# Kernel optimization log

Measured on AMD Instinct MI355X. Metric: run time of the kernel, lower is better.

Reference implementation:

```python
import jax, jax.numpy as jnp
import numpy as np

N = 100000
E = 1600000
IN_C = 128
HID = 128


def setup_inputs() -> dict:
    key = jax.random.key(0)
    ks = jax.random.split(key, 16)
    x = jax.random.normal(ks[0], (N, IN_C), dtype=jnp.float32)
    edge_index = jax.random.randint(ks[1], (2, E), 0, N, dtype=jnp.int64)

    def lin(k, fan_in, fan_out):
        kw, kb = jax.random.split(k)
        bound = 1.0 / np.sqrt(fan_in)
        w = jax.random.uniform(kw, (fan_in, fan_out), minval=-bound, maxval=bound, dtype=jnp.float32)
        b = jax.random.uniform(kb, (fan_out,), minval=-bound, maxval=bound, dtype=jnp.float32)
        return w, b

    w0a, b0a = lin(ks[2], IN_C, HID)
    w0b, b0b = lin(ks[3], HID, HID)
    w1a, b1a = lin(ks[4], HID, HID)
    w1b, b1b = lin(ks[5], HID, HID)
    w2a, b2a = lin(ks[6], HID, HID)
    w2b, b2b = lin(ks[7], HID, HID)
    lin_w, lin_b = lin(ks[8], HID, 1)
    return {
        "x": x, "edge_index": edge_index,
        "w0a": w0a, "b0a": b0a, "w0b": w0b, "b0b": b0b,
        "w1a": w1a, "b1a": b1a, "w1b": w1b, "b1b": b1b,
        "w2a": w2a, "b2a": b2a, "w2b": w2b, "b2b": b2b,
        "lin_w": lin_w, "lin_b": lin_b,
    }


def _gin_conv(x, src, dst, wa, ba, wb, bb):
    # scatter-add neighbor sum: agg[i] = sum_{(j,i) in edges} x[j]  (eps = 0)
    agg = jax.ops.segment_sum(x[src], dst, num_segments=N)
    h = x + agg
    h = jax.nn.relu(h @ wa + ba)
    return h @ wb + bb


def reference(x, edge_index, w0a, b0a, w0b, b0b, w1a, b1a, w1b, b1b,
              w2a, b2a, w2b, b2b, lin_w, lin_b):
    src, dst = edge_index[0], edge_index[1]
    # dropout is identity in eval mode
    h = jax.nn.elu(_gin_conv(x, src, dst, w0a, b0a, w0b, b0b))
    h = jax.nn.elu(_gin_conv(h, src, dst, w1a, b1a, w1b, b1b))
    h = jax.nn.elu(_gin_conv(h, src, dst, w2a, b2a, w2b, b2b))
    out = jax.nn.sigmoid(h @ lin_w + lin_b)
    return out.squeeze(-1)  # [N]
```

## Files before the change

### kernel.cpp

```cpp
#include <hip/hip_runtime.h>
#include <hip/hip_bf16.h>
#include <math.h>

#define NN 100000
#define CC 128
#define EE 1600000
#define EPT 8
#define FCHUNK (256 * EPT)
#define NCHUNKS ((EE + FCHUNK - 1) / FCHUNK)
#define NB_E NCHUNKS
#define WB 512
#define WSHIFT 9
#define NBUCK ((NN + WB - 1) / WB)

typedef short  bf16x8 __attribute__((ext_vector_type(8)));
typedef float  f32x4  __attribute__((ext_vector_type(4)));
typedef float  f32x4v __attribute__((ext_vector_type(4)));
typedef unsigned short u16x8 __attribute__((ext_vector_type(8)));

#define WPAD 136
#define TP   136
#define MLPB 256
#define MLPW 8

__device__ __forceinline__ ushort f2bf(float f) {
    __hip_bfloat16 h = __float2bfloat16(f);
    return __builtin_bit_cast(ushort, h);
}
__device__ __forceinline__ float bf2f(ushort u) {
    return __builtin_bit_cast(float, ((unsigned int)u) << 16);
}


__global__ void __launch_bounds__(256) bucket_hist(
    const int* __restrict__ dst, int* __restrict__ cnt)
{
    __shared__ int h[NBUCK];
    for (int i = threadIdx.x; i < NBUCK; i += 256) h[i] = 0;
    __syncthreads();
    int base = blockIdx.x * FCHUNK + threadIdx.x * EPT;
    if (base + EPT <= EE) {
        int4 d0 = *(const int4*)&dst[base];
        int4 d1 = *(const int4*)&dst[base + 4];
        int dd[8] = {d0.x, d0.y, d0.z, d0.w, d1.x, d1.y, d1.z, d1.w};
#pragma unroll
        for (int i = 0; i < 8; ++i) atomicAdd(&h[dd[i] >> WSHIFT], 1);
    } else {
        for (int i = 0; i < EPT; ++i) {
            int e = base + i;
            if (e < EE) atomicAdd(&h[dst[e] >> WSHIFT], 1);
        }
    }
    __syncthreads();
    for (int i = threadIdx.x; i < NBUCK; i += 256)
        cnt[i * NB_E + blockIdx.x] = h[i];
}

__global__ void __launch_bounds__(256) scan_cnt(
    int* __restrict__ cnt, int* __restrict__ total)
{
    __shared__ int wsum[4];
    int row = blockIdx.x;
    int* p = cnt + row * NB_E;
    int tid = threadIdx.x, lane = tid & 63, wid = tid >> 6;
    int v[4], s = 0;
#pragma unroll
    for (int j = 0; j < 4; ++j) {
        int idx = tid * 4 + j;
        v[j] = (idx < NB_E) ? p[idx] : 0;
        s += v[j];
    }
    int inc = s;
#pragma unroll
    for (int off = 1; off < 64; off <<= 1) {
        int n = __shfl_up(inc, off);
        if (lane >= off) inc += n;
    }
    if (lane == 63) wsum[wid] = inc;
    __syncthreads();
    int wofs = 0;
#pragma unroll
    for (int w = 0; w < 4; ++w)
        if (w < wid) wofs += wsum[w];
    int run = wofs + inc - s;
#pragma unroll
    for (int j = 0; j < 4; ++j) {
        int idx = tid * 4 + j;
        if (idx < NB_E) p[idx] = run;
        run += v[j];
    }
    if (tid == 255) total[row] = run;
}

__global__ void scan_base(const int* __restrict__ total,
                          int* __restrict__ bucketBase, int* __restrict__ rowptr)
{
    int lane = threadIdx.x;
    int v[4], s = 0;
#pragma unroll
    for (int j = 0; j < 4; ++j) {
        int idx = lane * 4 + j;
        v[j] = (idx < NBUCK) ? total[idx] : 0;
        s += v[j];
    }
    int inc = s;
#pragma unroll
    for (int off = 1; off < 64; off <<= 1) {
        int n = __shfl_up(inc, off);
        if (lane >= off) inc += n;
    }
    int run = inc - s;
#pragma unroll
    for (int j = 0; j < 4; ++j) {
        int idx = lane * 4 + j;
        if (idx < NBUCK) bucketBase[idx] = run;
        run += v[j];
    }
    if (lane == 63) { bucketBase[NBUCK] = EE; rowptr[NN] = EE; }
}

__global__ void __launch_bounds__(256) bucket_scatter(
    const int* __restrict__ src, const int* __restrict__ dst,
    const int* __restrict__ cntEx, const int* __restrict__ bucketBase,
    unsigned int* __restrict__ pairs)
{
    __shared__ int h[NBUCK];
    __shared__ int bOfs[NBUCK];
    for (int i = threadIdx.x; i < NBUCK; i += 256) {
        h[i] = 0;
        bOfs[i] = bucketBase[i] + cntEx[i * NB_E + blockIdx.x];
    }
    __syncthreads();
    int base = blockIdx.x * FCHUNK + threadIdx.x * EPT;
    if (base + EPT <= EE) {
        int4 d0 = *(const int4*)&dst[base];
        int4 d1 = *(const int4*)&dst[base + 4];
        int4 s0 = *(const int4*)&src[base];
        int4 s1 = *(const int4*)&src[base + 4];
        int dd[8] = {d0.x, d0.y, d0.z, d0.w, d1.x, d1.y, d1.z, d1.w};
        int ss[8] = {s0.x, s0.y, s0.z, s0.w, s1.x, s1.y, s1.z, s1.w};
#pragma unroll
        for (int i = 0; i < 8; ++i) {
            int d = dd[i];
            int k = d >> WSHIFT;
            int r = atomicAdd(&h[k], 1);
            pairs[bOfs[k] + r] = ((unsigned)ss[i] << WSHIFT) | (unsigned)(d & (WB - 1));
        }
    } else {
        for (int i = 0; i < EPT; ++i) {
            int e = base + i;
            if (e < EE) {
                int d = dst[e];
                int k = d >> WSHIFT;
                int r = atomicAdd(&h[k], 1);
                pairs[bOfs[k] + r] = ((unsigned)src[e] << WSHIFT) | (unsigned)(d & (WB - 1));
            }
        }
    }
}

__global__ void __launch_bounds__(256) csr_build(
    const unsigned int* __restrict__ pairs, const int* __restrict__ bucketBase,
    int* __restrict__ rowptr, int* __restrict__ col)
{
    __shared__ int cnt[WB];
    __shared__ int ofs[WB];
    __shared__ int wsum[4];
    int k = blockIdx.x;
    int tid = threadIdx.x, lane = tid & 63, wid = tid >> 6;
    int nodeBase = k * WB;
    int nNodes = NN - nodeBase; if (nNodes > WB) nNodes = WB;
    for (int i = tid; i < WB; i += 256) cnt[i] = 0;
    __syncthreads();
    int beg = bucketBase[k], end = bucketBase[k + 1];
    for (int e = beg + tid; e < end; e += 256)
        atomicAdd(&cnt[pairs[e] & (WB - 1)], 1);
    __syncthreads();
    int a = cnt[2 * tid], b = cnt[2 * tid + 1];
    int s = a + b;
    int inc = s;
#pragma unroll
    for (int off = 1; off < 64; off <<= 1) {
        int n = __shfl_up(inc, off);
        if (lane >= off) inc += n;
    }
    if (lane == 63) wsum[wid] = inc;
    __syncthreads();
    int wofs = 0;
#pragma unroll
    for (int w = 0; w < 4; ++w)
        if (w < wid) wofs += wsum[w];
    int excl = wofs + inc - s;
    ofs[2 * tid] = excl;
    ofs[2 * tid + 1] = excl + a;
    __syncthreads();
    for (int i = tid; i < nNodes; i += 256)
        rowptr[nodeBase + i] = beg + ofs[i];
    __syncthreads();
    for (int e = beg + tid; e < end; e += 256) {
        unsigned p = pairs[e];
        int dl = p & (WB - 1);
        int r = atomicAdd(&ofs[dl], 1);
        col[beg + r] = (int)(p >> WSHIFT);
    }
}

__global__ void __launch_bounds__(256) convert_x_kernel(
    const float* __restrict__ x, ushort* __restrict__ xb)
{
    int i = blockIdx.x * 256 + threadIdx.x;
    f32x4v v = __builtin_nontemporal_load((const f32x4v*)x + i);
    ushort4 o;
    o.x = f2bf(v[0]); o.y = f2bf(v[1]); o.z = f2bf(v[2]); o.w = f2bf(v[3]);
    ((ushort4*)xb)[i] = o;
}

__global__ void __launch_bounds__(256) convert_w6_kernel(
    const float* __restrict__ w0, const float* __restrict__ w1,
    const float* __restrict__ w2, const float* __restrict__ w3,
    const float* __restrict__ w4, const float* __restrict__ w5,
    ushort* __restrict__ wt)
{
    int i = blockIdx.x * 256 + threadIdx.x;
    int mat = i >> 14;
    int rem = i & 16383;
    int k = rem >> 7, n = rem & 127;
    const float* w = (mat == 0) ? w0 : (mat == 1) ? w1 : (mat == 2) ? w2
                   : (mat == 3) ? w3 : (mat == 4) ? w4 : w5;
    wt[mat * 16384 + n * 128 + k] = f2bf(w[k * 128 + n]);
}

__global__ void __launch_bounds__(256) gather_agg(
    const ushort* __restrict__ hin, const int* __restrict__ rowptr,
    const int* __restrict__ col, ushort* __restrict__ agg)
{
    const int grp    = threadIdx.x >> 4;
    const int lane16 = threadIdx.x & 15;
    const int gbase  = (threadIdx.x & 63) & 48;
    const int n = blockIdx.x * 16 + grp;
    const u16x8* hp = (const u16x8*)hin;

    u16x8 self = hp[n * 16 + lane16];
    float s0[8], s1[8], s2[8], s3[8];
#pragma unroll
    for (int k = 0; k < 8; ++k) {
        s0[k] = bf2f(self[k]); s1[k] = 0.f; s2[k] = 0.f; s3[k] = 0.f;
    }

    int beg = rowptr[n], end = rowptr[n + 1];
    while (beg < end) {
        int take = end - beg;
        if (take > 16) take = 16;
        int ci = (lane16 < take) ? col[beg + lane16] : 0;
        int j = 0;
        for (; j + 4 <= take; j += 4) {
            int n0 = __shfl(ci, gbase + j + 0);
            int n1 = __shfl(ci, gbase + j + 1);
            int n2 = __shfl(ci, gbase + j + 2);
            int n3 = __shfl(ci, gbase + j + 3);
            u16x8 a0 = hp[n0 * 16 + lane16];
            u16x8 a1 = hp[n1 * 16 + lane16];
            u16x8 a2 = hp[n2 * 16 + lane16];
            u16x8 a3 = hp[n3 * 16 + lane16];
#pragma unroll
            for (int k = 0; k < 8; ++k) {
                s0[k] += bf2f(a0[k]); s1[k] += bf2f(a1[k]);
                s2[k] += bf2f(a2[k]); s3[k] += bf2f(a3[k]);
            }
        }
        for (; j < take; ++j) {
            int n0 = __shfl(ci, gbase + j);
            u16x8 a0 = hp[n0 * 16 + lane16];
#pragma unroll
            for (int k = 0; k < 8; ++k) s0[k] += bf2f(a0[k]);
        }
        beg += take;
    }

    bf16x8 o;
#pragma unroll
    for (int k = 0; k < 8; ++k) o[k] = (short)f2bf(s0[k] + s1[k] + s2[k] + s3[k]);
    *(bf16x8*)&((ushort*)agg)[n * CC + lane16 * 8] = o;
}

template <bool FUSE_HEAD>
__global__ void __launch_bounds__(512, 2) mlp_persist(
    const ushort* __restrict__ hin,
    const ushort* __restrict__ waT, const float* __restrict__ ba,
    const ushort* __restrict__ wbT, const float* __restrict__ bb,
    ushort* __restrict__ hout,
    const float* __restrict__ lw, const float* __restrict__ lb,
    float* __restrict__ out)
{
    __shared__ ushort WaS[CC * WPAD];
    __shared__ ushort WbS[CC * WPAD];
    __shared__ ushort Tt[MLPW][16 * TP];
    __shared__ float  baS[CC], bbS[CC], lwS[CC];

    const int tid = threadIdx.x;

    for (int i = tid; i < CC * 16; i += 512) {
        int row = i >> 4, ch = i & 15;
        *(bf16x8*)&WaS[row * WPAD + ch * 8] = *(const bf16x8*)&waT[row * CC + ch * 8];
        *(bf16x8*)&WbS[row * WPAD + ch * 8] = *(const bf16x8*)&wbT[row * CC + ch * 8];
    }
    if (tid < CC)                    baS[tid]          = ba[tid];
    else if (tid < 2 * CC)           bbS[tid - CC]     = bb[tid - CC];
    else if (FUSE_HEAD && tid < 3 * CC) lwS[tid - 2 * CC] = lw[tid - 2 * CC];
    __syncthreads();

    const int wave = tid >> 6;
    const int lane = tid & 63;
    const int quad = lane >> 4;
    const int l16  = lane & 15;
    ushort* T = Tt[wave];
    const int nTiles = NN / 16;
    const int stride = MLPB * MLPW;

    int wv = blockIdx.x * MLPW + wave;
    if (wv >= nTiles) return;

    const int fq4 = quad * 4;
    float lbv = FUSE_HEAD ? lb[0] : 0.f;

    bf16x8 af[4];
#pragma unroll
    for (int kk = 0; kk < 4; ++kk)
        af[kk] = *(const bf16x8*)&hin[(wv * 16 + l16) * CC + kk * 32 + quad * 8];

    while (true) {
        const int wrow0 = wv * 16;
        const int wnext = wv + stride;

        bf16x8 afn[4];
        if (wnext < nTiles) {
#pragma unroll
            for (int kk = 0; kk < 4; ++kk)
                afn[kk] = *(const bf16x8*)&hin[(wnext * 16 + l16) * CC + kk * 32 + quad * 8];
        }

        ushort* Trow = &T[l16 * TP];

#pragma unroll
        for (int nt = 0; nt < 8; ++nt) {
            f32x4 a = *(const f32x4*)&baS[nt * 16 + fq4];
#pragma unroll
            for (int kk = 0; kk < 4; ++kk) {
                bf16x8 wfrag = *(const bf16x8*)&WaS[(nt * 16 + l16) * WPAD + kk * 32 + quad * 8];
                a = __builtin_amdgcn_mfma_f32_16x16x32_bf16(wfrag, af[kk], a, 0, 0, 0);
            }
            ushort4 pk;
            pk.x = f2bf(fmaxf(a[0], 0.f));
            pk.y = f2bf(fmaxf(a[1], 0.f));
            pk.z = f2bf(fmaxf(a[2], 0.f));
            pk.w = f2bf(fmaxf(a[3], 0.f));
            *(ushort4*)&Trow[nt * 16 + fq4] = pk;
        }
        __builtin_amdgcn_sched_barrier(0);

        bf16x8 tf[4];
#pragma unroll
        for (int kk = 0; kk < 4; ++kk)
            tf[kk] = *(const bf16x8*)&Trow[kk * 32 + quad * 8];
        __builtin_amdgcn_sched_barrier(0);

        if (FUSE_HEAD) {
            float part = 0.f;
#pragma unroll
            for (int nt = 0; nt < 8; ++nt) {
                f32x4 a2 = *(const f32x4*)&bbS[nt * 16 + fq4];
#pragma unroll
                for (int kk = 0; kk < 4; ++kk) {
                    bf16x8 wfrag = *(const bf16x8*)&WbS[(nt * 16 + l16) * WPAD + kk * 32 + quad * 8];
                    a2 = __builtin_amdgcn_mfma_f32_16x16x32_bf16(wfrag, tf[kk], a2, 0, 0, 0);
                }
                f32x4 lw4 = *(const f32x4*)&lwS[nt * 16 + fq4];
#pragma unroll
                for (int r = 0; r < 4; ++r) {
                    float v = a2[r];
                    v = v > 0.f ? v : expm1f(v);
                    part += v * lw4[r];
                }
            }
            part += __shfl_xor(part, 16);
            part += __shfl_xor(part, 32);
            if (lane < 16) {
                float z = part + lbv;
                out[wrow0 + l16] = 1.f / (1.f + expf(-z));
            }
        } else {
#pragma unroll
            for (int nt = 0; nt < 8; ++nt) {
                f32x4 a2 = *(const f32x4*)&bbS[nt * 16 + fq4];
#pragma unroll
                for (int kk = 0; kk < 4; ++kk) {
                    bf16x8 wfrag = *(const bf16x8*)&WbS[(nt * 16 + l16) * WPAD + kk * 32 + quad * 8];
                    a2 = __builtin_amdgcn_mfma_f32_16x16x32_bf16(wfrag, tf[kk], a2, 0, 0, 0);
                }
                ushort4 pk;
#pragma unroll
                for (int r = 0; r < 4; ++r) {
                    float v = a2[r];
                    v = v > 0.f ? v : expm1f(v);
                    ((ushort*)&pk)[r] = f2bf(v);
                }
                *(ushort4*)&Trow[nt * 16 + fq4] = pk;
            }
#pragma unroll
            for (int i = 0; i < 4; ++i) {
                int r = i * 4 + quad;
                bf16x8 o = *(const bf16x8*)&T[r * TP + l16 * 8];
                *(bf16x8*)&hout[(wrow0 + r) * CC + l16 * 8] = o;
            }
        }

        if (wnext >= nTiles) break;
        wv = wnext;
#pragma unroll
        for (int kk = 0; kk < 4; ++kk) af[kk] = afn[kk];
    }
}

extern "C" void kernel_launch(void* const* d_in, const int* in_sizes, int n_in,
                              void* d_out, int out_size, void* d_ws, size_t ws_size,
                              hipStream_t stream) {
    const float* x   = (const float*)d_in[0];
    const int*   ei  = (const int*)d_in[1];
    const int*   src = ei;
    const int*   dst = ei + EE;
    const float* w0a = (const float*)d_in[2];
    const float* b0a = (const float*)d_in[3];
    const float* w0b = (const float*)d_in[4];
    const float* b0b = (const float*)d_in[5];
    const float* w1a = (const float*)d_in[6];
    const float* b1a = (const float*)d_in[7];
    const float* w1b = (const float*)d_in[8];
    const float* b1b = (const float*)d_in[9];
    const float* w2a = (const float*)d_in[10];
    const float* b2a = (const float*)d_in[11];
    const float* w2b = (const float*)d_in[12];
    const float* b2b = (const float*)d_in[13];
    const float* lw  = (const float*)d_in[14];
    const float* lb  = (const float*)d_in[15];
    float* outp = (float*)d_out;

    ushort* xb  = (ushort*)d_ws;
    ushort* hbA = xb + (size_t)NN * CC;
    ushort* agg = hbA + (size_t)NN * CC;
    ushort* wT  = agg + (size_t)NN * CC;
    int* col    = (int*)(wT + 6 * CC * CC);
    int* rowptr = col + EE;

    unsigned int* pairs = (unsigned int*)agg;
    int* cnt        = (int*)(pairs + EE);
    int* total      = cnt + NBUCK * NB_E;
    int* bucketBase = total + NBUCK;

    ushort* w0aT = wT;
    ushort* w0bT = wT + 1 * CC * CC;
    ushort* w1aT = wT + 2 * CC * CC;
    ushort* w1bT = wT + 3 * CC * CC;
    ushort* w2aT = wT + 4 * CC * CC;
    ushort* w2bT = wT + 5 * CC * CC;

    const int gatherBlocks = NN / 16;
    const int cvtXBlocks   = (NN * CC / 4) / 256;

    convert_x_kernel<<<cvtXBlocks, 256, 0, stream>>>(x, xb);
    convert_w6_kernel<<<6 * 64, 256, 0, stream>>>(w0a, w0b, w1a, w1b, w2a, w2b, wT);

    bucket_hist<<<NB_E, 256, 0, stream>>>(dst, cnt);
    scan_cnt<<<NBUCK, 256, 0, stream>>>(cnt, total);
    scan_base<<<1, 64, 0, stream>>>(total, bucketBase, rowptr);
    bucket_scatter<<<NB_E, 256, 0, stream>>>(src, dst, cnt, bucketBase, pairs);
    csr_build<<<NBUCK, 256, 0, stream>>>(pairs, bucketBase, rowptr, col);

    gather_agg<<<gatherBlocks, 256, 0, stream>>>(xb, rowptr, col, agg);
    mlp_persist<false><<<MLPB, 512, 0, stream>>>(agg, w0aT, b0a, w0bT, b0b, hbA,
                                                 nullptr, nullptr, nullptr);
    gather_agg<<<gatherBlocks, 256, 0, stream>>>(hbA, rowptr, col, agg);
    mlp_persist<false><<<MLPB, 512, 0, stream>>>(agg, w1aT, b1a, w1bT, b1b, xb,
                                                 nullptr, nullptr, nullptr);
    gather_agg<<<gatherBlocks, 256, 0, stream>>>(xb, rowptr, col, agg);
    mlp_persist<true><<<MLPB, 512, 0, stream>>>(agg, w2aT, b2a, w2bT, b2b, nullptr,
                                                lw, lb, outp);
}
```

Measured before the change: 418.7 us.

## Fuse neighbor gather-aggregation with per-layer MLP into one kernel

Merges the gather_agg kernel and the persistent MLP kernel into a single gin_layer kernel. Each 256-thread block aggregates 16 nodes into LDS, then its four waves each compute two output column tiles of both MFMA matmuls, reading weights straight from global memory (L2-cached) instead of staging them in LDS. This removes the bf16 agg write and re-read to global memory and three kernel launches. In exchange, every block re-fetches the full weight matrices from cache, and there are more block-level barriers per tile.

```diff
diff --git a/kernel.cpp b/kernel.cpp
--- a/kernel.cpp
+++ b/kernel.cpp
@@ -18,10 +18,7 @@
 typedef float  f32x4v __attribute__((ext_vector_type(4)));
 typedef unsigned short u16x8 __attribute__((ext_vector_type(8)));
 
-#define WPAD 136
 #define TP   136
-#define MLPB 256
-#define MLPW 8
 
 __device__ __forceinline__ ushort f2bf(float f) {
     __hip_bfloat16 h = __float2bfloat16(f);
@@ -230,194 +227,156 @@
     wt[mat * 16384 + n * 128 + k] = f2bf(w[k * 128 + n]);
 }
 
-__global__ void __launch_bounds__(256) gather_agg(
+template <bool FUSE_HEAD>
+__global__ void __launch_bounds__(256, 4) gin_layer(
     const ushort* __restrict__ hin, const int* __restrict__ rowptr,
-    const int* __restrict__ col, ushort* __restrict__ agg)
-{
-    const int grp    = threadIdx.x >> 4;
-    const int lane16 = threadIdx.x & 15;
-    const int gbase  = (threadIdx.x & 63) & 48;
-    const int n = blockIdx.x * 16 + grp;
-    const u16x8* hp = (const u16x8*)hin;
-
-    u16x8 self = hp[n * 16 + lane16];
-    float s0[8], s1[8], s2[8], s3[8];
-#pragma unroll
-    for (int k = 0; k < 8; ++k) {
-        s0[k] = bf2f(self[k]); s1[k] = 0.f; s2[k] = 0.f; s3[k] = 0.f;
-    }
-
-    int beg = rowptr[n], end = rowptr[n + 1];
-    while (beg < end) {
-        int take = end - beg;
-        if (take > 16) take = 16;
-        int ci = (lane16 < take) ? col[beg + lane16] : 0;
-        int j = 0;
-        for (; j + 4 <= take; j += 4) {
-            int n0 = __shfl(ci, gbase + j + 0);
-            int n1 = __shfl(ci, gbase + j + 1);
-            int n2 = __shfl(ci, gbase + j + 2);
-            int n3 = __shfl(ci, gbase + j + 3);
-            u16x8 a0 = hp[n0 * 16 + lane16];
-            u16x8 a1 = hp[n1 * 16 + lane16];
-            u16x8 a2 = hp[n2 * 16 + lane16];
-            u16x8 a3 = hp[n3 * 16 + lane16];
-#pragma unroll
-            for (int k = 0; k < 8; ++k) {
-                s0[k] += bf2f(a0[k]); s1[k] += bf2f(a1[k]);
-                s2[k] += bf2f(a2[k]); s3[k] += bf2f(a3[k]);
-            }
-        }
-        for (; j < take; ++j) {
-            int n0 = __shfl(ci, gbase + j);
-            u16x8 a0 = hp[n0 * 16 + lane16];
-#pragma unroll
-            for (int k = 0; k < 8; ++k) s0[k] += bf2f(a0[k]);
-        }
-        beg += take;
-    }
-
-    bf16x8 o;
-#pragma unroll
-    for (int k = 0; k < 8; ++k) o[k] = (short)f2bf(s0[k] + s1[k] + s2[k] + s3[k]);
-    *(bf16x8*)&((ushort*)agg)[n * CC + lane16 * 8] = o;
-}
-
-template <bool FUSE_HEAD>
-__global__ void __launch_bounds__(512, 2) mlp_persist(
-    const ushort* __restrict__ hin,
+    const int* __restrict__ col,
     const ushort* __restrict__ waT, const float* __restrict__ ba,
     const ushort* __restrict__ wbT, const float* __restrict__ bb,
     ushort* __restrict__ hout,
     const float* __restrict__ lw, const float* __restrict__ lb,
     float* __restrict__ out)
 {
-    __shared__ ushort WaS[CC * WPAD];
-    __shared__ ushort WbS[CC * WPAD];
-    __shared__ ushort Tt[MLPW][16 * TP];
-    __shared__ float  baS[CC], bbS[CC], lwS[CC];
+    __shared__ ushort T0[16][TP];
+    __shared__ ushort T1[16][TP];
+    __shared__ float  headP[4][16];
 
     const int tid = threadIdx.x;
 
-    for (int i = tid; i < CC * 16; i += 512) {
-        int row = i >> 4, ch = i & 15;
-        *(bf16x8*)&WaS[row * WPAD + ch * 8] = *(const bf16x8*)&waT[row * CC + ch * 8];
-        *(bf16x8*)&WbS[row * WPAD + ch * 8] = *(const bf16x8*)&wbT[row * CC + ch * 8];
-    }
-    if (tid < CC)                    baS[tid]          = ba[tid];
-    else if (tid < 2 * CC)           bbS[tid - CC]     = bb[tid - CC];
-    else if (FUSE_HEAD && tid < 3 * CC) lwS[tid - 2 * CC] = lw[tid - 2 * CC];
+    {
+        const int grp  = tid >> 4;
+        const int g16  = tid & 15;
+        const int gbase = (tid & 63) & 48;
+        const int n = blockIdx.x * 16 + grp;
+        const u16x8* hp = (const u16x8*)hin;
+
+        u16x8 self = hp[n * 16 + g16];
+        float s0[8], s1[8], s2[8], s3[8];
+#pragma unroll
+        for (int k = 0; k < 8; ++k) {
+            s0[k] = bf2f(self[k]); s1[k] = 0.f; s2[k] = 0.f; s3[k] = 0.f;
+        }
+
+        int beg = rowptr[n], end = rowptr[n + 1];
+        while (beg < end) {
+            int take = end - beg;
+            if (take > 16) take = 16;
+            int ci = (g16 < take) ? col[beg + g16] : 0;
+            int j = 0;
+            for (; j + 4 <= take; j += 4) {
+                int n0 = __shfl(ci, gbase + j + 0);
+                int n1 = __shfl(ci, gbase + j + 1);
+                int n2 = __shfl(ci, gbase + j + 2);
+                int n3 = __shfl(ci, gbase + j + 3);
+                u16x8 a0 = hp[n0 * 16 + g16];
+                u16x8 a1 = hp[n1 * 16 + g16];
+                u16x8 a2 = hp[n2 * 16 + g16];
+                u16x8 a3 = hp[n3 * 16 + g16];
+#pragma unroll
+                for (int k = 0; k < 8; ++k) {
+                    s0[k] += bf2f(a0[k]); s1[k] += bf2f(a1[k]);
+                    s2[k] += bf2f(a2[k]); s3[k] += bf2f(a3[k]);
+                }
+            }
+            for (; j < take; ++j) {
+                int n0 = __shfl(ci, gbase + j);
+                u16x8 a0 = hp[n0 * 16 + g16];
+#pragma unroll
+                for (int k = 0; k < 8; ++k) s0[k] += bf2f(a0[k]);
+            }
+            beg += take;
+        }
+
+        bf16x8 o;
+#pragma unroll
+        for (int k = 0; k < 8; ++k) o[k] = (short)f2bf(s0[k] + s1[k] + s2[k] + s3[k]);
+        *(bf16x8*)&T0[grp][g16 * 8] = o;
+    }
     __syncthreads();
 
     const int wave = tid >> 6;
     const int lane = tid & 63;
     const int quad = lane >> 4;
     const int l16  = lane & 15;
-    ushort* T = Tt[wave];
-    const int nTiles = NN / 16;
-    const int stride = MLPB * MLPW;
-
-    int wv = blockIdx.x * MLPW + wave;
-    if (wv >= nTiles) return;
-
-    const int fq4 = quad * 4;
-    float lbv = FUSE_HEAD ? lb[0] : 0.f;
+    const int fq4  = quad * 4;
 
     bf16x8 af[4];
 #pragma unroll
     for (int kk = 0; kk < 4; ++kk)
-        af[kk] = *(const bf16x8*)&hin[(wv * 16 + l16) * CC + kk * 32 + quad * 8];
-
-    while (true) {
-        const int wrow0 = wv * 16;
-        const int wnext = wv + stride;
-
-        bf16x8 afn[4];
-        if (wnext < nTiles) {
-#pragma unroll
-            for (int kk = 0; kk < 4; ++kk)
-                afn[kk] = *(const bf16x8*)&hin[(wnext * 16 + l16) * CC + kk * 32 + quad * 8];
-        }
-
-        ushort* Trow = &T[l16 * TP];
-
-#pragma unroll
-        for (int nt = 0; nt < 8; ++nt) {
-            f32x4 a = *(const f32x4*)&baS[nt * 16 + fq4];
+        af[kk] = *(const bf16x8*)&T0[l16][kk * 32 + quad * 8];
+
+#pragma unroll
+    for (int t = 0; t < 2; ++t) {
+        const int nt = wave * 2 + t;
+        f32x4 a = *(const f32x4*)&ba[nt * 16 + fq4];
+#pragma unroll
+        for (int kk = 0; kk < 4; ++kk) {
+            bf16x8 wfrag = *(const bf16x8*)&waT[(nt * 16 + l16) * CC + kk * 32 + quad * 8];
+            a = __builtin_amdgcn_mfma_f32_16x16x32_bf16(wfrag, af[kk], a, 0, 0, 0);
+        }
+        ushort4 pk;
+        pk.x = f2bf(fmaxf(a[0], 0.f));
+        pk.y = f2bf(fmaxf(a[1], 0.f));
+        pk.z = f2bf(fmaxf(a[2], 0.f));
+        pk.w = f2bf(fmaxf(a[3], 0.f));
+        *(ushort4*)&T1[l16][nt * 16 + fq4] = pk;
+    }
+    __syncthreads();
+
+    bf16x8 tf[4];
+#pragma unroll
+    for (int kk = 0; kk < 4; ++kk)
+        tf[kk] = *(const bf16x8*)&T1[l16][kk * 32 + quad * 8];
+
+    if (FUSE_HEAD) {
+        float part = 0.f;
+#pragma unroll
+        for (int t = 0; t < 2; ++t) {
+            const int nt = wave * 2 + t;
+            f32x4 a2 = *(const f32x4*)&bb[nt * 16 + fq4];
 #pragma unroll
             for (int kk = 0; kk < 4; ++kk) {
-                bf16x8 wfrag = *(const bf16x8*)&WaS[(nt * 16 + l16) * WPAD + kk * 32 + quad * 8];
-                a = __builtin_amdgcn_mfma_f32_16x16x32_bf16(wfrag, af[kk], a, 0, 0, 0);
+                bf16x8 wfrag = *(const bf16x8*)&wbT[(nt * 16 + l16) * CC + kk * 32 + quad * 8];
+                a2 = __builtin_amdgcn_mfma_f32_16x16x32_bf16(wfrag, tf[kk], a2, 0, 0, 0);
+            }
+            f32x4 lw4 = *(const f32x4*)&lw[nt * 16 + fq4];
+#pragma unroll
+            for (int r = 0; r < 4; ++r) {
+                float v = a2[r];
+                v = v > 0.f ? v : expm1f(v);
+                part += v * lw4[r];
+            }
+        }
+        part += __shfl_xor(part, 16);
+        part += __shfl_xor(part, 32);
+        if (lane < 16) headP[wave][l16] = part;
+        __syncthreads();
+        if (tid < 16) {
+            float z = headP[0][tid] + headP[1][tid] + headP[2][tid] + headP[3][tid] + lb[0];
+            out[blockIdx.x * 16 + tid] = 1.f / (1.f + expf(-z));
+        }
+    } else {
+#pragma unroll
+        for (int t = 0; t < 2; ++t) {
+            const int nt = wave * 2 + t;
+            f32x4 a2 = *(const f32x4*)&bb[nt * 16 + fq4];
+#pragma unroll
+            for (int kk = 0; kk < 4; ++kk) {
+                bf16x8 wfrag = *(const bf16x8*)&wbT[(nt * 16 + l16) * CC + kk * 32 + quad * 8];
+                a2 = __builtin_amdgcn_mfma_f32_16x16x32_bf16(wfrag, tf[kk], a2, 0, 0, 0);
             }
             ushort4 pk;
-            pk.x = f2bf(fmaxf(a[0], 0.f));
-            pk.y = f2bf(fmaxf(a[1], 0.f));
-            pk.z = f2bf(fmaxf(a[2], 0.f));
-            pk.w = f2bf(fmaxf(a[3], 0.f));
-            *(ushort4*)&Trow[nt * 16 + fq4] = pk;
-        }
-        __builtin_amdgcn_sched_barrier(0);
-
-        bf16x8 tf[4];
-#pragma unroll
-        for (int kk = 0; kk < 4; ++kk)
-            tf[kk] = *(const bf16x8*)&Trow[kk * 32 + quad * 8];
-        __builtin_amdgcn_sched_barrier(0);
-
-        if (FUSE_HEAD) {
-            float part = 0.f;
-#pragma unroll
-            for (int nt = 0; nt < 8; ++nt) {
-                f32x4 a2 = *(const f32x4*)&bbS[nt * 16 + fq4];
-#pragma unroll
-                for (int kk = 0; kk < 4; ++kk) {
-                    bf16x8 wfrag = *(const bf16x8*)&WbS[(nt * 16 + l16) * WPAD + kk * 32 + quad * 8];
-                    a2 = __builtin_amdgcn_mfma_f32_16x16x32_bf16(wfrag, tf[kk], a2, 0, 0, 0);
-                }
-                f32x4 lw4 = *(const f32x4*)&lwS[nt * 16 + fq4];
-#pragma unroll
-                for (int r = 0; r < 4; ++r) {
-                    float v = a2[r];
-                    v = v > 0.f ? v : expm1f(v);
-                    part += v * lw4[r];
-                }
-            }
-            part += __shfl_xor(part, 16);
-            part += __shfl_xor(part, 32);
-            if (lane < 16) {
-                float z = part + lbv;
-                out[wrow0 + l16] = 1.f / (1.f + expf(-z));
-            }
-        } else {
-#pragma unroll
-            for (int nt = 0; nt < 8; ++nt) {
-                f32x4 a2 = *(const f32x4*)&bbS[nt * 16 + fq4];
-#pragma unroll
-                for (int kk = 0; kk < 4; ++kk) {
-                    bf16x8 wfrag = *(const bf16x8*)&WbS[(nt * 16 + l16) * WPAD + kk * 32 + quad * 8];
-                    a2 = __builtin_amdgcn_mfma_f32_16x16x32_bf16(wfrag, tf[kk], a2, 0, 0, 0);
-                }
-                ushort4 pk;
-#pragma unroll
-                for (int r = 0; r < 4; ++r) {
-                    float v = a2[r];
-                    v = v > 0.f ? v : expm1f(v);
-                    ((ushort*)&pk)[r] = f2bf(v);
-                }
-                *(ushort4*)&Trow[nt * 16 + fq4] = pk;
-            }
-#pragma unroll
-            for (int i = 0; i < 4; ++i) {
-                int r = i * 4 + quad;
-                bf16x8 o = *(const bf16x8*)&T[r * TP + l16 * 8];
-                *(bf16x8*)&hout[(wrow0 + r) * CC + l16 * 8] = o;
-            }
-        }
-
-        if (wnext >= nTiles) break;
-        wv = wnext;
-#pragma unroll
-        for (int kk = 0; kk < 4; ++kk) af[kk] = afn[kk];
+#pragma unroll
+            for (int r = 0; r < 4; ++r) {
+                float v = a2[r];
+                v = v > 0.f ? v : expm1f(v);
+                ((ushort*)&pk)[r] = f2bf(v);
+            }
+            *(ushort4*)&T0[l16][nt * 16 + fq4] = pk;
+        }
+        __syncthreads();
+        *(bf16x8*)&hout[(blockIdx.x * 16 + (tid >> 4)) * CC + (tid & 15) * 8] =
+            *(const bf16x8*)&T0[tid >> 4][(tid & 15) * 8];
     }
 }
 
@@ -446,12 +405,12 @@
 
     ushort* xb  = (ushort*)d_ws;
     ushort* hbA = xb + (size_t)NN * CC;
-    ushort* agg = hbA + (size_t)NN * CC;
-    ushort* wT  = agg + (size_t)NN * CC;
+    ushort* scr = hbA + (size_t)NN * CC;
+    ushort* wT  = scr + (size_t)NN * CC;
     int* col    = (int*)(wT + 6 * CC * CC);
     int* rowptr = col + EE;
 
-    unsigned int* pairs = (unsigned int*)agg;
+    unsigned int* pairs = (unsigned int*)scr;
     int* cnt        = (int*)(pairs + EE);
     int* total      = cnt + NBUCK * NB_E;
     int* bucketBase = total + NBUCK;
@@ -463,8 +422,8 @@
     ushort* w2aT = wT + 4 * CC * CC;
     ushort* w2bT = wT + 5 * CC * CC;
 
-    const int gatherBlocks = NN / 16;
-    const int cvtXBlocks   = (NN * CC / 4) / 256;
+    const int layerBlocks = NN / 16;
+    const int cvtXBlocks  = (NN * CC / 4) / 256;
 
     convert_x_kernel<<<cvtXBlocks, 256, 0, stream>>>(x, xb);
     convert_w6_kernel<<<6 * 64, 256, 0, stream>>>(w0a, w0b, w1a, w1b, w2a, w2b, wT);
@@ -475,13 +434,10 @@
     bucket_scatter<<<NB_E, 256, 0, stream>>>(src, dst, cnt, bucketBase, pairs);
     csr_build<<<NBUCK, 256, 0, stream>>>(pairs, bucketBase, rowptr, col);
 
-    gather_agg<<<gatherBlocks, 256, 0, stream>>>(xb, rowptr, col, agg);
-    mlp_persist<false><<<MLPB, 512, 0, stream>>>(agg, w0aT, b0a, w0bT, b0b, hbA,
-                                                 nullptr, nullptr, nullptr);
-    gather_agg<<<gatherBlocks, 256, 0, stream>>>(hbA, rowptr, col, agg);
-    mlp_persist<false><<<MLPB, 512, 0, stream>>>(agg, w1aT, b1a, w1bT, b1b, xb,
-                                                 nullptr, nullptr, nullptr);
-    gather_agg<<<gatherBlocks, 256, 0, stream>>>(xb, rowptr, col, agg);
-    mlp_persist<true><<<MLPB, 512, 0, stream>>>(agg, w2aT, b2a, w2bT, b2b, nullptr,
-                                                lw, lb, outp);
-}
+    gin_layer<false><<<layerBlocks, 256, 0, stream>>>(
+        xb, rowptr, col, w0aT, b0a, w0bT, b0b, hbA, nullptr, nullptr, nullptr);
+    gin_layer<false><<<layerBlocks, 256, 0, stream>>>(
+        hbA, rowptr, col, w1aT, b1a, w1bT, b1b, xb, nullptr, nullptr, nullptr);
+    gin_layer<true><<<layerBlocks, 256, 0, stream>>>(
+        xb, rowptr, col, w2aT, b2a, w2bT, b2b, nullptr, lw, lb, outp);
+}
```

Result: slower. 441.9 us (+5.5%).

## Fuse bucket histogram and scatter using fixed-capacity buckets with global atomics

Applied to the files above, without the earlier changes.

Replaces the histogram, per-block count scan and scatter passes with one kernel. It reserves per-bucket space through global atomics into fixed-capacity (PCAP) bucket slots, then scans the bucket totals for the CSR row offsets. This removes two kernel launches and one pass over dst. It relies on no bucket exceeding PCAP edges, which holds for uniform random inputs but could overflow on skewed graphs. The gather loop also gets an 8-wide unroll and a launch_bounds occupancy hint.

```diff
diff --git a/kernel.cpp b/kernel.cpp
--- a/kernel.cpp
+++ b/kernel.cpp
@@ -12,6 +12,7 @@
 #define WB 512
 #define WSHIFT 9
 #define NBUCK ((NN + WB - 1) / WB)
+#define PCAP 9216
 
 typedef short  bf16x8 __attribute__((ext_vector_type(8)));
 typedef float  f32x4  __attribute__((ext_vector_type(4)));
@@ -32,135 +33,94 @@
 }
 
 
-__global__ void __launch_bounds__(256) bucket_hist(
-    const int* __restrict__ dst, int* __restrict__ cnt)
-{
-    __shared__ int h[NBUCK];
-    for (int i = threadIdx.x; i < NBUCK; i += 256) h[i] = 0;
-    __syncthreads();
-    int base = blockIdx.x * FCHUNK + threadIdx.x * EPT;
-    if (base + EPT <= EE) {
-        int4 d0 = *(const int4*)&dst[base];
-        int4 d1 = *(const int4*)&dst[base + 4];
-        int dd[8] = {d0.x, d0.y, d0.z, d0.w, d1.x, d1.y, d1.z, d1.w};
-#pragma unroll
-        for (int i = 0; i < 8; ++i) atomicAdd(&h[dd[i] >> WSHIFT], 1);
-    } else {
-        for (int i = 0; i < EPT; ++i) {
-            int e = base + i;
-            if (e < EE) atomicAdd(&h[dst[e] >> WSHIFT], 1);
-        }
-    }
-    __syncthreads();
-    for (int i = threadIdx.x; i < NBUCK; i += 256)
-        cnt[i * NB_E + blockIdx.x] = h[i];
-}
-
-__global__ void __launch_bounds__(256) scan_cnt(
-    int* __restrict__ cnt, int* __restrict__ total)
-{
-    __shared__ int wsum[4];
-    int row = blockIdx.x;
-    int* p = cnt + row * NB_E;
-    int tid = threadIdx.x, lane = tid & 63, wid = tid >> 6;
-    int v[4], s = 0;
-#pragma unroll
-    for (int j = 0; j < 4; ++j) {
-        int idx = tid * 4 + j;
-        v[j] = (idx < NB_E) ? p[idx] : 0;
-        s += v[j];
-    }
-    int inc = s;
-#pragma unroll
-    for (int off = 1; off < 64; off <<= 1) {
-        int n = __shfl_up(inc, off);
-        if (lane >= off) inc += n;
-    }
-    if (lane == 63) wsum[wid] = inc;
-    __syncthreads();
-    int wofs = 0;
-#pragma unroll
-    for (int w = 0; w < 4; ++w)
-        if (w < wid) wofs += wsum[w];
-    int run = wofs + inc - s;
-#pragma unroll
-    for (int j = 0; j < 4; ++j) {
-        int idx = tid * 4 + j;
-        if (idx < NB_E) p[idx] = run;
-        run += v[j];
-    }
-    if (tid == 255) total[row] = run;
-}
-
-__global__ void scan_base(const int* __restrict__ total,
-                          int* __restrict__ bucketBase, int* __restrict__ rowptr)
-{
-    int lane = threadIdx.x;
-    int v[4], s = 0;
-#pragma unroll
-    for (int j = 0; j < 4; ++j) {
-        int idx = lane * 4 + j;
-        v[j] = (idx < NBUCK) ? total[idx] : 0;
-        s += v[j];
-    }
-    int inc = s;
-#pragma unroll
-    for (int off = 1; off < 64; off <<= 1) {
-        int n = __shfl_up(inc, off);
-        if (lane >= off) inc += n;
-    }
-    int run = inc - s;
-#pragma unroll
-    for (int j = 0; j < 4; ++j) {
-        int idx = lane * 4 + j;
-        if (idx < NBUCK) bucketBase[idx] = run;
-        run += v[j];
-    }
-    if (lane == 63) { bucketBase[NBUCK] = EE; rowptr[NN] = EE; }
-}
-
-__global__ void __launch_bounds__(256) bucket_scatter(
+__global__ void __launch_bounds__(256) bucket_scatter_fused(
     const int* __restrict__ src, const int* __restrict__ dst,
-    const int* __restrict__ cntEx, const int* __restrict__ bucketBase,
-    unsigned int* __restrict__ pairs)
+    int* __restrict__ bucketCur, unsigned int* __restrict__ pairs)
 {
     __shared__ int h[NBUCK];
     __shared__ int bOfs[NBUCK];
-    for (int i = threadIdx.x; i < NBUCK; i += 256) {
-        h[i] = 0;
-        bOfs[i] = bucketBase[i] + cntEx[i * NB_E + blockIdx.x];
-    }
-    __syncthreads();
-    int base = blockIdx.x * FCHUNK + threadIdx.x * EPT;
+    const int tid = threadIdx.x;
+    for (int i = tid; i < NBUCK; i += 256) h[i] = 0;
+    __syncthreads();
+
+    int base = blockIdx.x * FCHUNK + tid * EPT;
+    int dd[8], ss[8], rr[8];
     if (base + EPT <= EE) {
         int4 d0 = *(const int4*)&dst[base];
         int4 d1 = *(const int4*)&dst[base + 4];
         int4 s0 = *(const int4*)&src[base];
         int4 s1 = *(const int4*)&src[base + 4];
-        int dd[8] = {d0.x, d0.y, d0.z, d0.w, d1.x, d1.y, d1.z, d1.w};
-        int ss[8] = {s0.x, s0.y, s0.z, s0.w, s1.x, s1.y, s1.z, s1.w};
-#pragma unroll
-        for (int i = 0; i < 8; ++i) {
-            int d = dd[i];
-            int k = d >> WSHIFT;
-            int r = atomicAdd(&h[k], 1);
-            pairs[bOfs[k] + r] = ((unsigned)ss[i] << WSHIFT) | (unsigned)(d & (WB - 1));
-        }
+        dd[0]=d0.x; dd[1]=d0.y; dd[2]=d0.z; dd[3]=d0.w;
+        dd[4]=d1.x; dd[5]=d1.y; dd[6]=d1.z; dd[7]=d1.w;
+        ss[0]=s0.x; ss[1]=s0.y; ss[2]=s0.z; ss[3]=s0.w;
+        ss[4]=s1.x; ss[5]=s1.y; ss[6]=s1.z; ss[7]=s1.w;
+#pragma unroll
+        for (int i = 0; i < 8; ++i)
+            rr[i] = atomicAdd(&h[dd[i] >> WSHIFT], 1);
     } else {
+#pragma unroll
+        for (int i = 0; i < 8; ++i) { dd[i] = 0; ss[i] = 0; rr[i] = -1; }
         for (int i = 0; i < EPT; ++i) {
             int e = base + i;
             if (e < EE) {
-                int d = dst[e];
-                int k = d >> WSHIFT;
-                int r = atomicAdd(&h[k], 1);
-                pairs[bOfs[k] + r] = ((unsigned)src[e] << WSHIFT) | (unsigned)(d & (WB - 1));
-            }
-        }
-    }
+                dd[i] = dst[e]; ss[i] = src[e];
+                rr[i] = atomicAdd(&h[dd[i] >> WSHIFT], 1);
+            }
+        }
+    }
+    __syncthreads();
+    for (int i = tid; i < NBUCK; i += 256)
+        bOfs[i] = (h[i] > 0) ? atomicAdd(&bucketCur[i], h[i]) : 0;
+    __syncthreads();
+
+    if (base + EPT <= EE) {
+#pragma unroll
+        for (int i = 0; i < 8; ++i) {
+            int k = dd[i] >> WSHIFT;
+            pairs[(size_t)k * PCAP + bOfs[k] + rr[i]] =
+                ((unsigned)ss[i] << WSHIFT) | (unsigned)(dd[i] & (WB - 1));
+        }
+    } else {
+        for (int i = 0; i < EPT; ++i) {
+            if (rr[i] >= 0) {
+                int k = dd[i] >> WSHIFT;
+                pairs[(size_t)k * PCAP + bOfs[k] + rr[i]] =
+                    ((unsigned)ss[i] << WSHIFT) | (unsigned)(dd[i] & (WB - 1));
+            }
+        }
+    }
+}
+
+__global__ void scan_base(const int* __restrict__ bucketCur,
+                          int* __restrict__ bucketBase, int* __restrict__ rowptr)
+{
+    int lane = threadIdx.x;
+    int v[4], s = 0;
+#pragma unroll
+    for (int j = 0; j < 4; ++j) {
+        int idx = lane * 4 + j;
+        v[j] = (idx < NBUCK) ? bucketCur[idx] : 0;
+        s += v[j];
+    }
+    int inc = s;
+#pragma unroll
+    for (int off = 1; off < 64; off <<= 1) {
+        int n = __shfl_up(inc, off);
+        if (lane >= off) inc += n;
+    }
+    int run = inc - s;
+#pragma unroll
+    for (int j = 0; j < 4; ++j) {
+        int idx = lane * 4 + j;
+        if (idx < NBUCK) bucketBase[idx] = run;
+        run += v[j];
+    }
+    if (lane == 63) rowptr[NN] = EE;
 }
 
 __global__ void __launch_bounds__(256) csr_build(
-    const unsigned int* __restrict__ pairs, const int* __restrict__ bucketBase,
+    const unsigned int* __restrict__ pairs, const int* __restrict__ bucketCur,
+    const int* __restrict__ bucketBase,
     int* __restrict__ rowptr, int* __restrict__ col)
 {
     __shared__ int cnt[WB];
@@ -172,9 +132,11 @@
     int nNodes = NN - nodeBase; if (nNodes > WB) nNodes = WB;
     for (int i = tid; i < WB; i += 256) cnt[i] = 0;
     __syncthreads();
-    int beg = bucketBase[k], end = bucketBase[k + 1];
-    for (int e = beg + tid; e < end; e += 256)
-        atomicAdd(&cnt[pairs[e] & (WB - 1)], 1);
+    const unsigned int* p = pairs + (size_t)k * PCAP;
+    int total = bucketCur[k];
+    int begW = bucketBase[k];
+    for (int e = tid; e < total; e += 256)
+        atomicAdd(&cnt[p[e] & (WB - 1)], 1);
     __syncthreads();
     int a = cnt[2 * tid], b = cnt[2 * tid + 1];
     int s = a + b;
@@ -195,24 +157,25 @@
     ofs[2 * tid + 1] = excl + a;
     __syncthreads();
     for (int i = tid; i < nNodes; i += 256)
-        rowptr[nodeBase + i] = beg + ofs[i];
-    __syncthreads();
-    for (int e = beg + tid; e < end; e += 256) {
-        unsigned p = pairs[e];
-        int dl = p & (WB - 1);
+        rowptr[nodeBase + i] = begW + ofs[i];
+    __syncthreads();
+    for (int e = tid; e < total; e += 256) {
+        unsigned pv = p[e];
+        int dl = pv & (WB - 1);
         int r = atomicAdd(&ofs[dl], 1);
-        col[beg + r] = (int)(p >> WSHIFT);
+        col[begW + r] = (int)(pv >> WSHIFT);
     }
 }
 
 __global__ void __launch_bounds__(256) convert_x_kernel(
-    const float* __restrict__ x, ushort* __restrict__ xb)
+    const float* __restrict__ x, ushort* __restrict__ xb, int* __restrict__ bucketCur)
 {
     int i = blockIdx.x * 256 + threadIdx.x;
     f32x4v v = __builtin_nontemporal_load((const f32x4v*)x + i);
     ushort4 o;
     o.x = f2bf(v[0]); o.y = f2bf(v[1]); o.z = f2bf(v[2]); o.w = f2bf(v[3]);
     ((ushort4*)xb)[i] = o;
+    if (i < NBUCK) bucketCur[i] = 0;
 }
 
 __global__ void __launch_bounds__(256) convert_w6_kernel(
@@ -230,7 +193,7 @@
     wt[mat * 16384 + n * 128 + k] = f2bf(w[k * 128 + n]);
 }
 
-__global__ void __launch_bounds__(256) gather_agg(
+__global__ void __launch_bounds__(256, 4) gather_agg(
     const ushort* __restrict__ hin, const int* __restrict__ rowptr,
     const int* __restrict__ col, ushort* __restrict__ agg)
 {
@@ -253,6 +216,31 @@
         if (take > 16) take = 16;
         int ci = (lane16 < take) ? col[beg + lane16] : 0;
         int j = 0;
+        for (; j + 8 <= take; j += 8) {
+            int n0 = __shfl(ci, gbase + j + 0);
+            int n1 = __shfl(ci, gbase + j + 1);
+            int n2 = __shfl(ci, gbase + j + 2);
+            int n3 = __shfl(ci, gbase + j + 3);
+            int n4 = __shfl(ci, gbase + j + 4);
+            int n5 = __shfl(ci, gbase + j + 5);
+            int n6 = __shfl(ci, gbase + j + 6);
+            int n7 = __shfl(ci, gbase + j + 7);
+            u16x8 a0 = hp[n0 * 16 + lane16];
+            u16x8 a1 = hp[n1 * 16 + lane16];
+            u16x8 a2 = hp[n2 * 16 + lane16];
+            u16x8 a3 = hp[n3 * 16 + lane16];
+            u16x8 a4 = hp[n4 * 16 + lane16];
+            u16x8 a5 = hp[n5 * 16 + lane16];
+            u16x8 a6 = hp[n6 * 16 + lane16];
+            u16x8 a7 = hp[n7 * 16 + lane16];
+#pragma unroll
+            for (int k = 0; k < 8; ++k) {
+                s0[k] += bf2f(a0[k]) + bf2f(a4[k]);
+                s1[k] += bf2f(a1[k]) + bf2f(a5[k]);
+                s2[k] += bf2f(a2[k]) + bf2f(a6[k]);
+                s3[k] += bf2f(a3[k]) + bf2f(a7[k]);
+            }
+        }
         for (; j + 4 <= take; j += 4) {
             int n0 = __shfl(ci, gbase + j + 0);
             int n1 = __shfl(ci, gbase + j + 1);
@@ -450,11 +438,10 @@
     ushort* wT  = agg + (size_t)NN * CC;
     int* col    = (int*)(wT + 6 * CC * CC);
     int* rowptr = col + EE;
+    int* bucketCur  = rowptr + NN + 1;
+    int* bucketBase = bucketCur + NBUCK;
 
     unsigned int* pairs = (unsigned int*)agg;
-    int* cnt        = (int*)(pairs + EE);
-    int* total      = cnt + NBUCK * NB_E;
-    int* bucketBase = total + NBUCK;
 
     ushort* w0aT = wT;
     ushort* w0bT = wT + 1 * CC * CC;
@@ -466,14 +453,12 @@
     const int gatherBlocks = NN / 16;
     const int cvtXBlocks   = (NN * CC / 4) / 256;
 
-    convert_x_kernel<<<cvtXBlocks, 256, 0, stream>>>(x, xb);
+    convert_x_kernel<<<cvtXBlocks, 256, 0, stream>>>(x, xb, bucketCur);
     convert_w6_kernel<<<6 * 64, 256, 0, stream>>>(w0a, w0b, w1a, w1b, w2a, w2b, wT);
 
-    bucket_hist<<<NB_E, 256, 0, stream>>>(dst, cnt);
-    scan_cnt<<<NBUCK, 256, 0, stream>>>(cnt, total);
-    scan_base<<<1, 64, 0, stream>>>(total, bucketBase, rowptr);
-    bucket_scatter<<<NB_E, 256, 0, stream>>>(src, dst, cnt, bucketBase, pairs);
-    csr_build<<<NBUCK, 256, 0, stream>>>(pairs, bucketBase, rowptr, col);
+    bucket_scatter_fused<<<NB_E, 256, 0, stream>>>(src, dst, bucketCur, pairs);
+    scan_base<<<1, 64, 0, stream>>>(bucketCur, bucketBase, rowptr);
+    csr_build<<<NBUCK, 256, 0, stream>>>(pairs, bucketCur, bucketBase, rowptr, col);
 
     gather_agg<<<gatherBlocks, 256, 0, stream>>>(xb, rowptr, col, agg);
     mlp_persist<false><<<MLPB, 512, 0, stream>>>(agg, w0aT, b0a, w0bT, b0b, hbA,
```

After: 434.2 us. 3.7% more time.

## Replace persistent LDS-weight MLP with per-tile blocks reading weights from global

Applied to the files above, without the earlier changes.

The persistent MLP kernel, which staged both 128x128 bf16 weight matrices in LDS and looped over tiles with prefetch, becomes a non-persistent kernel launching one block per 8 tiles of 16 rows. Weight fragments are now loaded straight from global memory, expected to hit in L1/L2, on every MFMA step. This drops the per-block LDS weight staging and cuts LDS use, which could raise occupancy. The cost is repeated global/cache weight loads in the inner loop and no cross-tile prefetch of activations.

```diff
diff --git a/kernel.cpp b/kernel.cpp
--- a/kernel.cpp
+++ b/kernel.cpp
@@ -18,10 +18,7 @@
 typedef float  f32x4v __attribute__((ext_vector_type(4)));
 typedef unsigned short u16x8 __attribute__((ext_vector_type(8)));
 
-#define WPAD 136
 #define TP   136
-#define MLPB 256
-#define MLPW 8
 
 __device__ __forceinline__ ushort f2bf(float f) {
     __hip_bfloat16 h = __float2bfloat16(f);
@@ -284,7 +281,7 @@
 }
 
 template <bool FUSE_HEAD>
-__global__ void __launch_bounds__(512, 2) mlp_persist(
+__global__ void __launch_bounds__(512, 2) mlp_tile(
     const ushort* __restrict__ hin,
     const ushort* __restrict__ waT, const float* __restrict__ ba,
     const ushort* __restrict__ wbT, const float* __restrict__ bb,
@@ -292,132 +289,102 @@
     const float* __restrict__ lw, const float* __restrict__ lb,
     float* __restrict__ out)
 {
-    __shared__ ushort WaS[CC * WPAD];
-    __shared__ ushort WbS[CC * WPAD];
-    __shared__ ushort Tt[MLPW][16 * TP];
+    __shared__ ushort Tt[8][16 * TP];
     __shared__ float  baS[CC], bbS[CC], lwS[CC];
 
     const int tid = threadIdx.x;
-
-    for (int i = tid; i < CC * 16; i += 512) {
-        int row = i >> 4, ch = i & 15;
-        *(bf16x8*)&WaS[row * WPAD + ch * 8] = *(const bf16x8*)&waT[row * CC + ch * 8];
-        *(bf16x8*)&WbS[row * WPAD + ch * 8] = *(const bf16x8*)&wbT[row * CC + ch * 8];
-    }
-    if (tid < CC)                    baS[tid]          = ba[tid];
-    else if (tid < 2 * CC)           bbS[tid - CC]     = bb[tid - CC];
-    else if (FUSE_HEAD && tid < 3 * CC) lwS[tid - 2 * CC] = lw[tid - 2 * CC];
+    if (tid < CC)                       baS[tid]           = ba[tid];
+    else if (tid < 2 * CC)              bbS[tid - CC]      = bb[tid - CC];
+    else if (FUSE_HEAD && tid < 3 * CC) lwS[tid - 2 * CC]  = lw[tid - 2 * CC];
     __syncthreads();
 
     const int wave = tid >> 6;
     const int lane = tid & 63;
     const int quad = lane >> 4;
     const int l16  = lane & 15;
-    ushort* T = Tt[wave];
-    const int nTiles = NN / 16;
-    const int stride = MLPB * MLPW;
-
-    int wv = blockIdx.x * MLPW + wave;
-    if (wv >= nTiles) return;
-
-    const int fq4 = quad * 4;
-    float lbv = FUSE_HEAD ? lb[0] : 0.f;
+    const int fq4  = quad * 4;
+
+    const int wv = blockIdx.x * 8 + wave;
+    if (wv >= NN / 16) return;
+    const int wrow0 = wv * 16;
+    ushort* Trow = &Tt[wave][l16 * TP];
 
     bf16x8 af[4];
 #pragma unroll
     for (int kk = 0; kk < 4; ++kk)
-        af[kk] = *(const bf16x8*)&hin[(wv * 16 + l16) * CC + kk * 32 + quad * 8];
-
-    while (true) {
-        const int wrow0 = wv * 16;
-        const int wnext = wv + stride;
-
-        bf16x8 afn[4];
-        if (wnext < nTiles) {
-#pragma unroll
-            for (int kk = 0; kk < 4; ++kk)
-                afn[kk] = *(const bf16x8*)&hin[(wnext * 16 + l16) * CC + kk * 32 + quad * 8];
-        }
-
-        ushort* Trow = &T[l16 * TP];
-
+        af[kk] = *(const bf16x8*)&hin[(wrow0 + l16) * CC + kk * 32 + quad * 8];
+
+#pragma unroll
+    for (int nt = 0; nt < 8; ++nt) {
+        f32x4 a = *(const f32x4*)&baS[nt * 16 + fq4];
+#pragma unroll
+        for (int kk = 0; kk < 4; ++kk) {
+            bf16x8 wfrag = *(const bf16x8*)&waT[(nt * 16 + l16) * CC + kk * 32 + quad * 8];
+            a = __builtin_amdgcn_mfma_f32_16x16x32_bf16(wfrag, af[kk], a, 0, 0, 0);
+        }
+        ushort4 pk;
+        pk.x = f2bf(fmaxf(a[0], 0.f));
+        pk.y = f2bf(fmaxf(a[1], 0.f));
+        pk.z = f2bf(fmaxf(a[2], 0.f));
+        pk.w = f2bf(fmaxf(a[3], 0.f));
+        *(ushort4*)&Trow[nt * 16 + fq4] = pk;
+    }
+    __builtin_amdgcn_sched_barrier(0);
+
+    bf16x8 tf[4];
+#pragma unroll
+    for (int kk = 0; kk < 4; ++kk)
+        tf[kk] = *(const bf16x8*)&Trow[kk * 32 + quad * 8];
+    __builtin_amdgcn_sched_barrier(0);
+
+    if (FUSE_HEAD) {
+        float part = 0.f;
 #pragma unroll
         for (int nt = 0; nt < 8; ++nt) {
-            f32x4 a = *(const f32x4*)&baS[nt * 16 + fq4];
+            f32x4 a2 = *(const f32x4*)&bbS[nt * 16 + fq4];
 #pragma unroll
             for (int kk = 0; kk < 4; ++kk) {
-                bf16x8 wfrag = *(const bf16x8*)&WaS[(nt * 16 + l16) * WPAD + kk * 32 + quad * 8];
-                a = __builtin_amdgcn_mfma_f32_16x16x32_bf16(wfrag, af[kk], a, 0, 0, 0);
+                bf16x8 wfrag = *(const bf16x8*)&wbT[(nt * 16 + l16) * CC + kk * 32 + quad * 8];
+                a2 = __builtin_amdgcn_mfma_f32_16x16x32_bf16(wfrag, tf[kk], a2, 0, 0, 0);
+            }
+            f32x4 lw4 = *(const f32x4*)&lwS[nt * 16 + fq4];
+#pragma unroll
+            for (int r = 0; r < 4; ++r) {
+                float v = a2[r];
+                v = v > 0.f ? v : expm1f(v);
+                part += v * lw4[r];
+            }
+        }
+        part += __shfl_xor(part, 16);
+        part += __shfl_xor(part, 32);
+        if (lane < 16) {
+            float z = part + lb[0];
+            out[wrow0 + l16] = 1.f / (1.f + expf(-z));
+        }
+    } else {
+#pragma unroll
+        for (int nt = 0; nt < 8; ++nt) {
+            f32x4 a2 = *(const f32x4*)&bbS[nt * 16 + fq4];
+#pragma unroll
+            for (int kk = 0; kk < 4; ++kk) {
+                bf16x8 wfrag = *(const bf16x8*)&wbT[(nt * 16 + l16) * CC + kk * 32 + quad * 8];
+                a2 = __builtin_amdgcn_mfma_f32_16x16x32_bf16(wfrag, tf[kk], a2, 0, 0, 0);
             }
             ushort4 pk;
-            pk.x = f2bf(fmaxf(a[0], 0.f));
-            pk.y = f2bf(fmaxf(a[1], 0.f));
-            pk.z = f2bf(fmaxf(a[2], 0.f));
-            pk.w = f2bf(fmaxf(a[3], 0.f));
+#pragma unroll
+            for (int r = 0; r < 4; ++r) {
+                float v = a2[r];
+                v = v > 0.f ? v : expm1f(v);
+                ((ushort*)&pk)[r] = f2bf(v);
+            }
             *(ushort4*)&Trow[nt * 16 + fq4] = pk;
         }
-        __builtin_amdgcn_sched_barrier(0);
-
-        bf16x8 tf[4];
-#pragma unroll
-        for (int kk = 0; kk < 4; ++kk)
-            tf[kk] = *(const bf16x8*)&Trow[kk * 32 + quad * 8];
-        __builtin_amdgcn_sched_barrier(0);
-
-        if (FUSE_HEAD) {
-            float part = 0.f;
-#pragma unroll
-            for (int nt = 0; nt < 8; ++nt) {
-                f32x4 a2 = *(const f32x4*)&bbS[nt * 16 + fq4];
-#pragma unroll
-                for (int kk = 0; kk < 4; ++kk) {
-                    bf16x8 wfrag = *(const bf16x8*)&WbS[(nt * 16 + l16) * WPAD + kk * 32 + quad * 8];
-                    a2 = __builtin_amdgcn_mfma_f32_16x16x32_bf16(wfrag, tf[kk], a2, 0, 0, 0);
-                }
-                f32x4 lw4 = *(const f32x4*)&lwS[nt * 16 + fq4];
-#pragma unroll
-                for (int r = 0; r < 4; ++r) {
-                    float v = a2[r];
-                    v = v > 0.f ? v : expm1f(v);
-                    part += v * lw4[r];
-                }
-            }
-            part += __shfl_xor(part, 16);
-            part += __shfl_xor(part, 32);
-            if (lane < 16) {
-                float z = part + lbv;
-                out[wrow0 + l16] = 1.f / (1.f + expf(-z));
-            }
-        } else {
-#pragma unroll
-            for (int nt = 0; nt < 8; ++nt) {
-                f32x4 a2 = *(const f32x4*)&bbS[nt * 16 + fq4];
-#pragma unroll
-                for (int kk = 0; kk < 4; ++kk) {
-                    bf16x8 wfrag = *(const bf16x8*)&WbS[(nt * 16 + l16) * WPAD + kk * 32 + quad * 8];
-                    a2 = __builtin_amdgcn_mfma_f32_16x16x32_bf16(wfrag, tf[kk], a2, 0, 0, 0);
-                }
-                ushort4 pk;
-#pragma unroll
-                for (int r = 0; r < 4; ++r) {
-                    float v = a2[r];
-                    v = v > 0.f ? v : expm1f(v);
-                    ((ushort*)&pk)[r] = f2bf(v);
-                }
-                *(ushort4*)&Trow[nt * 16 + fq4] = pk;
-            }
-#pragma unroll
-            for (int i = 0; i < 4; ++i) {
-                int r = i * 4 + quad;
-                bf16x8 o = *(const bf16x8*)&T[r * TP + l16 * 8];
-                *(bf16x8*)&hout[(wrow0 + r) * CC + l16 * 8] = o;
-            }
-        }
-
-        if (wnext >= nTiles) break;
-        wv = wnext;
-#pragma unroll
-        for (int kk = 0; kk < 4; ++kk) af[kk] = afn[kk];
+#pragma unroll
+        for (int i = 0; i < 4; ++i) {
+            int r = i * 4 + quad;
+            bf16x8 o = *(const bf16x8*)&Tt[wave][r * TP + l16 * 8];
+            *(bf16x8*)&hout[(wrow0 + r) * CC + l16 * 8] = o;
+        }
     }
 }
 
@@ -464,6 +431,7 @@
     ushort* w2bT = wT + 5 * CC * CC;
 
     const int gatherBlocks = NN / 16;
+    const int mlpBlocks    = (NN / 16 + 7) / 8;
     const int cvtXBlocks   = (NN * CC / 4) / 256;
 
     convert_x_kernel<<<cvtXBlocks, 256, 0, stream>>>(x, xb);
@@ -476,12 +444,12 @@
     csr_build<<<NBUCK, 256, 0, stream>>>(pairs, bucketBase, rowptr, col);
 
     gather_agg<<<gatherBlocks, 256, 0, stream>>>(xb, rowptr, col, agg);
-    mlp_persist<false><<<MLPB, 512, 0, stream>>>(agg, w0aT, b0a, w0bT, b0b, hbA,
-                                                 nullptr, nullptr, nullptr);
+    mlp_tile<false><<<mlpBlocks, 512, 0, stream>>>(agg, w0aT, b0a, w0bT, b0b, hbA,
+                                                   nullptr, nullptr, nullptr);
     gather_agg<<<gatherBlocks, 256, 0, stream>>>(hbA, rowptr, col, agg);
-    mlp_persist<false><<<MLPB, 512, 0, stream>>>(agg, w1aT, b1a, w1bT, b1b, xb,
-                                                 nullptr, nullptr, nullptr);
+    mlp_tile<false><<<mlpBlocks, 512, 0, stream>>>(agg, w1aT, b1a, w1bT, b1b, xb,
+                                                   nullptr, nullptr, nullptr);
     gather_agg<<<gatherBlocks, 256, 0, stream>>>(xb, rowptr, col, agg);
-    mlp_persist<true><<<MLPB, 512, 0, stream>>>(agg, w2aT, b2a, w2bT, b2b, nullptr,
-                                                lw, lb, outp);
-}
+    mlp_tile<true><<<mlpBlocks, 512, 0, stream>>>(agg, w2aT, b2a, w2bT, b2b, nullptr,
+                                                  lw, lb, outp);
+}
```

Result: slower. 532.4 us (+27.2%).
